# Performance work log

Measured on AMD Instinct MI355X. Metric: run time of the kernel, lower is better.

The kernel has to match this reference:

```python
import jax, jax.numpy as jnp
import numpy as np

K_NEIGHBORS = 8

def _cdist(x, y):
    x2 = jnp.sum(x * x, axis=-1)[:, None]
    y2 = jnp.sum(y * y, axis=-1)[None, :]
    d2 = x2 + y2 - 2.0 * (x @ y.T)
    return jnp.sqrt(jnp.maximum(d2, 0.0))

def setup_inputs() -> dict:
    key = jax.random.key(0)
    ks = jax.random.split(key, 16)
    B, C, H, W = 8, 384, 64, 64
    s = lambda fan: 1.0 / np.sqrt(fan)
    inp = {
        'fea': jax.random.normal(ks[0], (B, C, H, W), dtype=jnp.float32),
        # GCNConv weights (applied as x @ W) and post-aggregation biases
        'W1': jax.random.normal(ks[1], (C, C), jnp.float32) * s(C),
        'b1': jnp.zeros((C,), jnp.float32),
        'W2': jax.random.normal(ks[2], (C, C), jnp.float32) * s(C),
        'b2': jnp.zeros((C,), jnp.float32),
        'W3': jax.random.normal(ks[3], (C, C), jnp.float32) * s(C),
        'b3': jnp.zeros((C,), jnp.float32),
        # uncertainty MLP: C -> C/2 -> C/4 -> 1
        'U1': jax.random.normal(ks[4], (C, C // 2), jnp.float32) * s(C),
        'ub1': jnp.zeros((C // 2,), jnp.float32),
        'U2': jax.random.normal(ks[5], (C // 2, C // 4), jnp.float32) * s(C // 2),
        'ub2': jnp.zeros((C // 4,), jnp.float32),
        'U3': jax.random.normal(ks[6], (C // 4, 1), jnp.float32) * s(C // 4),
        'ub3': jnp.zeros((1,), jnp.float32),
    }
    return inp

def _build_graph(fea, k):
    B, C, H, W = fea.shape
    N = H * W
    gy, gx = jnp.meshgrid(jnp.arange(H), jnp.arange(W), indexing='ij')
    coord = jnp.stack([gy, gx], axis=-1).astype(jnp.float32).reshape(N, 2)
    fea_mean = fea.reshape(B, C, N).transpose(0, 2, 1).mean(0)  # [N, C]
    spatial_dist = _cdist(coord, coord)
    feature_dist = _cdist(fea_mean, fea_mean)
    combined = 0.7 * spatial_dist + 0.3 * feature_dist
    _, topk_idx = jax.lax.top_k(-combined, k)  # smallest-k per row
    src = jnp.repeat(jnp.arange(N), k)         # edge_index[0]
    dst = topk_idx.reshape(-1)                 # edge_index[1]
    return src, dst, N

def _gcn_conv(x, W, b, src, dst, N):
    # PyG GCNConv with symmetric normalization; self-loops are guaranteed
    # by construction (diag of combined dist is 0, strictly minimal), so
    # add_remaining_self_loops is a no-op.
    xw = x @ W                                              # [B, N, C]
    deg = jnp.zeros((N,), x.dtype).at[dst].add(1.0)
    dinv = jax.lax.rsqrt(deg)
    norm = dinv[src] * dinv[dst]                            # [E]
    msgs = xw[:, src, :] * norm[None, :, None]              # [B, E, C]
    out = jnp.zeros_like(xw).at[:, dst, :].add(msgs)
    return out + b

def reference(fea, W1, b1, W2, b2, W3, b3, U1, ub1, U2, ub2, U3, ub3):
    B, C, H, W = fea.shape
    src, dst, N = _build_graph(fea, K_NEIGHBORS)
    x = fea.reshape(B, C, N).transpose(0, 2, 1)             # [B, N, C]
    x = x + jax.nn.relu(_gcn_conv(x, W1, b1, src, dst, N))
    x = x + jax.nn.relu(_gcn_conv(x, W2, b2, src, dst, N))
    x = x + jax.nn.relu(_gcn_conv(x, W3, b3, src, dst, N))
    h = jax.nn.gelu(x @ U1 + ub1)
    h = jax.nn.gelu(h @ U2 + ub2)
    unc = jax.nn.sigmoid(h @ U3 + ub3)                      # [B, N, 1]
    unc = unc.reshape(B, 1, H, W)
    return fea * (1.0 + unc)
```

## Files before the change

### kernel.cpp

```cpp
#include <hip/hip_runtime.h>
#include <hip/hip_bf16.h>
#include <math.h>

#define N_NODES 4096
#define C_DIM   384
#define B_DIM   8
#define K_NB    8
#define E_TOT   (N_NODES * K_NB)
#define M_ROWS  (B_DIM * N_NODES)
#define NCHUNK  4
#define SROW    40

typedef unsigned long long u64;
typedef unsigned short u16;
typedef __attribute__((ext_vector_type(8))) short bf16x8;
typedef __attribute__((ext_vector_type(4))) float f32x4;
#define KEY_INF 0xFFFFFFFFFFFFFFFFull

__device__ __forceinline__ u16 f2bf(float f) {
  unsigned u = __float_as_uint(f);
  u += 0x7FFFu + ((u >> 16) & 1u);
  return (u16)(u >> 16);
}
__device__ __forceinline__ float bf2f(u16 h) {
  return __uint_as_float((unsigned)h << 16);
}
__device__ __forceinline__ f32x4 mfma16(bf16x8 a, bf16x8 b, f32x4 c) {
  return __builtin_amdgcn_mfma_f32_16x16x32_bf16(a, b, c, 0, 0, 0);
}
__device__ __forceinline__ void gl_lds16(const u16* gp, u16* lp) {
  __builtin_amdgcn_global_load_lds(
      (const __attribute__((address_space(1))) unsigned int*)gp,
      (__attribute__((address_space(3))) unsigned int*)lp, 16, 0, 0);
}

__device__ __forceinline__ void ce(u64& a, u64& b) {
  u64 lo = a < b ? a : b;
  u64 hi = a < b ? b : a;
  a = lo; b = hi;
}
__device__ __forceinline__ void ins8(u64 key, u64 (&r)[8]) {
  if (key < r[7]) {
    #pragma unroll
    for (int i = 0; i < 8; i++) {
      u64 lo = key < r[i] ? key : r[i];
      u64 hi = key < r[i] ? r[i] : key;
      r[i] = lo; key = hi;
    }
  }
}
__device__ __forceinline__ void merge8(u64 (&r)[8], const u64 (&o)[8]) {
  u64 c[8];
  #pragma unroll
  for (int i = 0; i < 8; i++) c[i] = r[i] < o[7 - i] ? r[i] : o[7 - i];
  ce(c[0], c[4]); ce(c[1], c[5]); ce(c[2], c[6]); ce(c[3], c[7]);
  ce(c[0], c[2]); ce(c[1], c[3]); ce(c[4], c[6]); ce(c[5], c[7]);
  ce(c[0], c[1]); ce(c[2], c[3]); ce(c[4], c[5]); ce(c[6], c[7]);
  #pragma unroll
  for (int i = 0; i < 8; i++) r[i] = c[i];
}

__global__ __launch_bounds__(256) void k_prep_w(
    const float* __restrict__ W1, const float* __restrict__ W2,
    const float* __restrict__ W3, const float* __restrict__ U1,
    const float* __restrict__ U2,
    u16* __restrict__ Wt1, u16* __restrict__ Wt2, u16* __restrict__ Wt3,
    u16* __restrict__ U1t, u16* __restrict__ U2t) {
  int idx = blockIdx.x * 256 + threadIdx.x;
  if (idx < 147456) {
    int n = idx / 384, k = idx % 384;
    Wt1[idx] = f2bf(W1[k * 384 + n]);
  } else if (idx < 294912) {
    int i = idx - 147456; int n = i / 384, k = i % 384;
    Wt2[i] = f2bf(W2[k * 384 + n]);
  } else if (idx < 442368) {
    int i = idx - 294912; int n = i / 384, k = i % 384;
    Wt3[i] = f2bf(W3[k * 384 + n]);
  } else if (idx < 516096) {
    int i = idx - 442368; int n = i / 384, k = i % 384;
    U1t[i] = f2bf(U1[k * 192 + n]);
  } else if (idx < 534528) {
    int i = idx - 516096; int n = i / 192, k = i % 192;
    U2t[i] = f2bf(U2[k * 96 + n]);
  }
}

__global__ __launch_bounds__(256) void k_transpose_mean(
    const float* __restrict__ fea, u16* __restrict__ Xb,
    u16* __restrict__ fh, u16* __restrict__ fl) {
  __shared__ float tb[32][132];
  __shared__ float ac[32][132];
  int n0 = blockIdx.x * 128, c0 = blockIdx.y * 32;
  int tx = threadIdx.x, ty = threadIdx.y;
  for (int i = ty; i < 32; i += 8) {
    #pragma unroll
    for (int e = 0; e < 4; e++) ac[i][tx * 4 + e] = 0.0f;
  }
  __syncthreads();
  for (int b = 0; b < B_DIM; b++) {
    for (int i = ty; i < 32; i += 8) {
      float4 v = *(const float4*)(fea +
          ((size_t)b * C_DIM + (c0 + i)) * N_NODES + n0 + tx * 4);
      *(float4*)&tb[i][tx * 4] = v;
      ac[i][tx * 4 + 0] += v.x;
      ac[i][tx * 4 + 1] += v.y;
      ac[i][tx * 4 + 2] += v.z;
      ac[i][tx * 4 + 3] += v.w;
    }
    __syncthreads();
    for (int rr = ty; rr < 128; rr += 8) {
      size_t o = ((size_t)b * N_NODES + (n0 + rr)) * C_DIM + c0 + tx;
      Xb[o] = f2bf(tb[tx][rr]);
    }
    __syncthreads();
  }
  for (int rr = ty; rr < 128; rr += 8) {
    float m = ac[tx][rr] * 0.125f;
    u16 h = f2bf(m);
    size_t o = (size_t)(n0 + rr) * C_DIM + c0 + tx;
    fh[o] = h;
    fl[o] = f2bf(m - bf2f(h));
  }
}

__global__ __launch_bounds__(64) void k_x2(const u16* __restrict__ fh,
                                           const u16* __restrict__ fl,
                                           float* __restrict__ x2) {
  int n = blockIdx.x;
  int lane = threadIdx.x;
  const u16* rh = fh + (size_t)n * C_DIM;
  const u16* rl = fl + (size_t)n * C_DIM;
  float s = 0.0f;
  for (int c = lane; c < C_DIM; c += 64) {
    float v = bf2f(rh[c]) + bf2f(rl[c]);
    s += v * v;
  }
  for (int d = 32; d > 0; d >>= 1) s += __shfl_down(s, d);
  if (lane == 0) x2[n] = s;
}

__global__ __launch_bounds__(256) void k_dist_win(
    const u16* __restrict__ fh, const u16* __restrict__ fl,
    const float* __restrict__ x2, u64* __restrict__ pk,
    int* __restrict__ deg, int* __restrict__ cnt) {
  __shared__ u16 WH[400 * SROW];
  __shared__ u16 WL[400 * SROW];
  int t = threadIdx.x;
  int lane = t & 63, w = t >> 6;
  int p = blockIdx.x;
  int py = p >> 4, px = p & 15;
  int iy0 = py * 4, ix0 = px * 4;
  int l15 = lane & 15;
  int kb = (lane >> 4) * 8;

  if (p < 16) { deg[p * 256 + t] = 0; cnt[p * 256 + t] = 0; }

  int t0 = (w == 0) ? 0 : 7 + (w - 1) * 6;
  int nt = w ? 6 : 7;

  int jj[7]; float x2j[7]; int jy_[7], jx_[7];
  #pragma unroll
  for (int tt = 0; tt < 7; tt++) {
    int s = (t0 + tt) * 16 + l15;
    int sy = s / 20, sx = s - sy * 20;
    int jy = iy0 - 8 + sy, jx = ix0 - 8 + sx;
    bool v = (tt < nt) && ((unsigned)jy < 64u) && ((unsigned)jx < 64u);
    jj[tt] = v ? (jy * 64 + jx) : -1;
    jy_[tt] = jy; jx_[tt] = jx;
    x2j[tt] = v ? x2[jy * 64 + jx] : 0.0f;
  }
  int pr = 168 + (l15 >> 2) * 20 + (l15 & 3);

  int seg = t & 3;
  int rb = t >> 2;

  f32x4 acc[7];
  #pragma unroll
  for (int tt = 0; tt < 7; tt++) acc[tt] = (f32x4){0.f, 0.f, 0.f, 0.f};

  for (int kc = 0; kc < 12; kc++) {
    int k0 = kc * 32;
    __syncthreads();
    #pragma unroll
    for (int it = 0; it < 7; it++) {
      int r = rb + 64 * it;
      if (r < 400) {
        int sy = r / 20, sx = r - sy * 20;
        int jy = iy0 - 8 + sy, jx = ix0 - 8 + sx;
        int j = (((unsigned)jy < 64u) && ((unsigned)jx < 64u)) ? jy * 64 + jx : 0;
        size_t src = (size_t)j * C_DIM + k0 + seg * 8;
        *(bf16x8*)&WH[r * SROW + seg * 8] = *(const bf16x8*)(fh + src);
        *(bf16x8*)&WL[r * SROW + seg * 8] = *(const bf16x8*)(fl + src);
      }
    }
    __syncthreads();
    bf16x8 aH = *(const bf16x8*)&WH[pr * SROW + kb];
    bf16x8 aL = *(const bf16x8*)&WL[pr * SROW + kb];
    #pragma unroll
    for (int tt = 0; tt < 7; tt++) {
      int row = (t0 + tt) * 16 + l15;
      bf16x8 bH = *(const bf16x8*)&WH[row * SROW + kb];
      bf16x8 bL = *(const bf16x8*)&WL[row * SROW + kb];
      acc[tt] = mfma16(aH, bH, acc[tt]);
      acc[tt] = mfma16(aL, bH, acc[tt]);
      acc[tt] = mfma16(aH, bL, acc[tt]);
    }
  }

  #pragma unroll
  for (int r = 0; r < 4; r++) {
    int r16 = ((lane >> 4) << 2) + r;
    int iy = iy0 + (r16 >> 2), ix = ix0 + (r16 & 3);
    int i = iy * 64 + ix;
    float x2i = x2[i];
    u64 top[8];
    #pragma unroll
    for (int q = 0; q < 8; q++) top[q] = KEY_INF;
    #pragma unroll
    for (int tt = 0; tt < 7; tt++) {
      float d2 = x2i + x2j[tt] - 2.0f * acc[tt][r];
      float fd = sqrtf(fmaxf(d2, 0.0f));
      float dy = (float)(iy - jy_[tt]), dx = (float)(ix - jx_[tt]);
      float sd = sqrtf(dy * dy + dx * dx);
      float comb = 0.7f * sd + 0.3f * fd;
      u64 key = (jj[tt] >= 0)
                    ? (((u64)__float_as_uint(comb) << 12) | (u64)jj[tt])
                    : KEY_INF;
      ins8(key, top);
    }
    #pragma unroll
    for (int d = 1; d < 16; d <<= 1) {
      u64 o[8];
      #pragma unroll
      for (int q = 0; q < 8; q++) o[q] = __shfl_xor(top[q], d);
      merge8(top, o);
    }
    if (l15 == 0) {
      #pragma unroll
      for (int q = 0; q < 8; q++)
        pk[((size_t)w * N_NODES + i) * 8 + q] = top[q];
    }
  }
}

__global__ __launch_bounds__(256) void k_topk_merge(
    const u64* __restrict__ pk, int* __restrict__ tk, int* __restrict__ flag,
    int* __restrict__ deg) {
  int n = blockIdx.x * 256 + threadIdx.x;
  if (n >= N_NODES) return;
  u64 r[8];
  #pragma unroll
  for (int q = 0; q < 8; q++) r[q] = KEY_INF;
  for (int c = 0; c < NCHUNK; c++) {
    const u64* lst = pk + ((size_t)c * N_NODES + n) * 8;
    #pragma unroll
    for (int q = 0; q < 8; q++) {
      u64 key = lst[q];
      if (key >= r[7]) break;
      ins8(key, r);
    }
  }
  float c8 = __uint_as_float((unsigned)(r[7] >> 12));
  int fl = (c8 > 6.28f) ? 1 : 0;
  flag[n] = fl;
  #pragma unroll
  for (int o = 0; o < 8; o++) {
    int idx = (int)(r[o] & 0xFFF);
    tk[n * 8 + o] = idx;
    if (!fl) atomicAdd(&deg[idx], 1);
  }
}

__global__ __launch_bounds__(256) void k_fb(
    const u16* __restrict__ fh, const u16* __restrict__ fl,
    const float* __restrict__ x2, const int* __restrict__ flag,
    int* __restrict__ tk, int* __restrict__ deg) {
  int w = threadIdx.x >> 6, lane = threadIdx.x & 63;
  for (int rr = 0; rr < 16; rr++) {
    int n = blockIdx.x * 64 + w * 16 + rr;
    if (!flag[n]) continue;
    u64 top[8];
    #pragma unroll
    for (int q = 0; q < 8; q++) top[q] = KEY_INF;
    float x2i = x2[n];
    int iy = n >> 6, ix = n & 63;
    const u16* rh = fh + (size_t)n * C_DIM;
    const u16* rl = fl + (size_t)n * C_DIM;
    for (int jb = 0; jb < N_NODES; jb += 64) {
      int j = jb + lane;
      const u16* ch = fh + (size_t)j * C_DIM;
      const u16* cl = fl + (size_t)j * C_DIM;
      float dot = 0.0f;
      for (int k2 = 0; k2 < C_DIM; k2++)
        dot += (bf2f(rh[k2]) + bf2f(rl[k2])) * (bf2f(ch[k2]) + bf2f(cl[k2]));
      float d2 = x2i + x2[j] - 2.0f * dot;
      float fd = sqrtf(fmaxf(d2, 0.0f));
      float dy = (float)(iy - (j >> 6)), dx = (float)(ix - (j & 63));
      float sd = sqrtf(dy * dy + dx * dx);
      float comb = 0.7f * sd + 0.3f * fd;
      ins8(((u64)__float_as_uint(comb) << 12) | (u64)j, top);
    }
    #pragma unroll
    for (int d = 1; d < 64; d <<= 1) {
      u64 o[8];
      #pragma unroll
      for (int q = 0; q < 8; q++) o[q] = __shfl_xor(top[q], d);
      merge8(top, o);
    }
    if (lane == 0) {
      #pragma unroll
      for (int q = 0; q < 8; q++) {
        int idx = (int)(top[q] & 0xFFF);
        tk[n * 8 + q] = idx;
        atomicAdd(&deg[idx], 1);
      }
    }
  }
}

__global__ __launch_bounds__(256) void k_scan(const int* __restrict__ deg,
                                              int* __restrict__ offs,
                                              float* __restrict__ dinv) {
  __shared__ int ps[256];
  int t = threadIdx.x;
  int base = t * 16;
  int loc[16]; int s = 0;
  for (int i = 0; i < 16; i++) { int d = deg[base + i]; loc[i] = s; s += d; }
  ps[t] = s;
  __syncthreads();
  for (int d = 1; d < 256; d <<= 1) {
    int add = (t >= d) ? ps[t - d] : 0;
    __syncthreads();
    ps[t] += add;
    __syncthreads();
  }
  int cbase = (t == 0) ? 0 : ps[t - 1];
  for (int i = 0; i < 16; i++) offs[base + i] = cbase + loc[i];
  if (t == 255) offs[N_NODES] = ps[255];
  for (int i = 0; i < 16; i++)
    dinv[base + i] = 1.0f / sqrtf((float)deg[base + i]);
}

__global__ __launch_bounds__(256) void k_fill(const int* __restrict__ tk,
                                              const int* __restrict__ offs,
                                              int* __restrict__ cnt,
                                              int* __restrict__ insrc) {
  int e = blockIdx.x * 256 + threadIdx.x;
  if (e >= E_TOT) return;
  int i = e >> 3;
  int n = tk[e];
  int pos = offs[n] + atomicAdd(&cnt[n], 1);
  insrc[pos] = i;
}

__global__ __launch_bounds__(256) void k_sort(const int* __restrict__ offs,
                                              int* __restrict__ insrc) {
  int n = blockIdx.x * 256 + threadIdx.x;
  if (n >= N_NODES) return;
  int beg = offs[n], end = offs[n + 1];
  for (int a = beg + 1; a < end; a++) {
    int v = insrc[a]; int p = a;
    while (p > beg && insrc[p - 1] > v) { insrc[p] = insrc[p - 1]; p--; }
    insrc[p] = v;
  }
}

__device__ __forceinline__ float gelu_f(float x) {
  const float k0 = 0.7978845608028654f;
  float x3 = x * x * x;
  return 0.5f * x * (1.0f + tanhf(k0 * (x + 0.044715f * x3)));
}

template <int EPI>
__global__ __launch_bounds__(256) void k_gemm_lds(
    const u16* __restrict__ A, const u16* __restrict__ Bt,
    const float* __restrict__ bias, u16* __restrict__ Cout,
    int M, int N, int K) {
  __shared__ u16 As[128 * 32];
  __shared__ u16 Bs[128 * 32];
  int t = threadIdx.x, lane = t & 63, w = t >> 6;
  int m0 = blockIdx.x * 128;
  int n0 = blockIdx.y * 128;
  int l15 = lane & 15;
  int kg = lane >> 4;
  int wr = (w >> 1) * 64, wc = (w & 1) * 64;

  int srow = w * 32 + (lane >> 2);
  int scol = (lane & 3) * 8;
  const u16* gA0 = A + (size_t)(m0 + srow) * K + scol;
  const u16* gA1 = A + (size_t)(m0 + srow + 16) * K + scol;
  int br0 = n0 + srow;      br0 = (br0 < N) ? br0 : 0;
  int br1 = n0 + srow + 16; br1 = (br1 < N) ? br1 : 0;
  const u16* gB0 = Bt + (size_t)br0 * K + scol;
  const u16* gB1 = Bt + (size_t)br1 * K + scol;
  u16* lA0 = &As[(w * 32) * 32];
  u16* lA1 = &As[(w * 32 + 16) * 32];
  u16* lB0 = &Bs[(w * 32) * 32];
  u16* lB1 = &Bs[(w * 32 + 16) * 32];

  f32x4 acc[4][4];
  #pragma unroll
  for (int s = 0; s < 4; s++)
    #pragma unroll
    for (int nt = 0; nt < 4; nt++) acc[s][nt] = (f32x4){0.f, 0.f, 0.f, 0.f};

  for (int kt = 0; kt < K; kt += 32) {
    __syncthreads();
    gl_lds16(gA0 + kt, lA0);
    gl_lds16(gA1 + kt, lA1);
    gl_lds16(gB0 + kt, lB0);
    gl_lds16(gB1 + kt, lB1);
    __syncthreads();
    bf16x8 a[4], b[4];
    #pragma unroll
    for (int s = 0; s < 4; s++)
      a[s] = *(const bf16x8*)&As[(wr + s * 16 + l15) * 32 + kg * 8];
    #pragma unroll
    for (int nt = 0; nt < 4; nt++)
      b[nt] = *(const bf16x8*)&Bs[(wc + nt * 16 + l15) * 32 + kg * 8];
    #pragma unroll
    for (int s = 0; s < 4; s++)
      #pragma unroll
      for (int nt = 0; nt < 4; nt++)
        acc[s][nt] = mfma16(a[s], b[nt], acc[s][nt]);
  }

  #pragma unroll
  for (int s = 0; s < 4; s++) {
    int rbase = m0 + wr + s * 16 + ((lane >> 4) << 2);
    #pragma unroll
    for (int nt = 0; nt < 4; nt++) {
      int n = n0 + wc + nt * 16 + l15;
      if (n >= N) continue;
      float bb = (EPI == 1) ? bias[n] : 0.0f;
      #pragma unroll
      for (int r = 0; r < 4; r++) {
        int m = rbase + r;
        float v = acc[s][nt][r];
        if (EPI == 1) { v += bb; v = gelu_f(v); }
        Cout[(size_t)m * N + n] = f2bf(v);
      }
    }
  }
}

__global__ __launch_bounds__(256) void k_mlp2(
    const u16* __restrict__ A, const u16* __restrict__ Bt,
    const float* __restrict__ ub2, const float* __restrict__ U3,
    const float* __restrict__ ub3, float* __restrict__ unc) {
  const int K = 192;
  int t = threadIdx.x, lane = t & 63, w = t >> 6;
  int m0 = blockIdx.x * 128 + w * 32;
  int l15 = lane & 15;
  int kb = (lane >> 4) * 8;

  f32x4 acc[2][6];
  #pragma unroll
  for (int s = 0; s < 2; s++)
    #pragma unroll
    for (int nt = 0; nt < 6; nt++) acc[s][nt] = (f32x4){0.f, 0.f, 0.f, 0.f};

  const u16* ap = A + (size_t)(m0 + l15) * K + kb;
  const u16* bp[6];
  #pragma unroll
  for (int nt = 0; nt < 6; nt++)
    bp[nt] = Bt + (size_t)(nt * 16 + l15) * K + kb;
  const size_t RA = (size_t)16 * K;

  #pragma unroll
  for (int kk = 0; kk < K; kk += 32) {
    bf16x8 a[2], b[6];
    #pragma unroll
    for (int s = 0; s < 2; s++) a[s] = *(const bf16x8*)(ap + s * RA + kk);
    #pragma unroll
    for (int nt = 0; nt < 6; nt++) b[nt] = *(const bf16x8*)(bp[nt] + kk);
    #pragma unroll
    for (int s = 0; s < 2; s++)
      #pragma unroll
      for (int nt = 0; nt < 6; nt++)
        acc[s][nt] = mfma16(a[s], b[nt], acc[s][nt]);
  }

  float ub3v = ub3[0];
  float u3v[6], b2v[6];
  #pragma unroll
  for (int nt = 0; nt < 6; nt++) {
    int col = nt * 16 + l15;
    u3v[nt] = U3[col];
    b2v[nt] = ub2[col];
  }
  #pragma unroll
  for (int s = 0; s < 2; s++) {
    #pragma unroll
    for (int r = 0; r < 4; r++) {
      float part = 0.0f;
      #pragma unroll
      for (int nt = 0; nt < 6; nt++)
        part += gelu_f(acc[s][nt][r] + b2v[nt]) * u3v[nt];
      #pragma unroll
      for (int d = 1; d < 16; d <<= 1) part += __shfl_xor(part, d);
      if (l15 == 0) {
        int m = m0 + s * 16 + ((lane >> 4) << 2) + r;
        unc[m] = 1.0f / (1.0f + expf(-(part + ub3v)));
      }
    }
  }
}

__global__ __launch_bounds__(384) void k_gcn_agg(
    const u16* __restrict__ xw, u16* __restrict__ Xb,
    const float* __restrict__ bias, const float* __restrict__ dinv,
    const int* __restrict__ offs, const int* __restrict__ insrc) {
  const size_t PLANE = (size_t)N_NODES * C_DIM;
  int t = threadIdx.x;
  int g = t / 48, l = t % 48;
  int slot = blockIdx.x * 8 + g;
  int n = slot >> 1;
  int hb = (slot & 1) * 4;
  int beg = offs[n], end = offs[n + 1];
  int c0 = l * 8;
  const u16* base = xw + c0 + (size_t)hb * PLANE;

  float a0[8] = {}, a1[8] = {}, a2[8] = {}, a3[8] = {};
  for (int e = beg; e < end; e++) {
    int i = insrc[e];
    float dv = dinv[i];
    const u16* rp = base + (size_t)i * C_DIM;
    bf16x8 v0 = *(const bf16x8*)(rp);
    bf16x8 v1 = *(const bf16x8*)(rp + PLANE);
    bf16x8 v2 = *(const bf16x8*)(rp + 2 * PLANE);
    bf16x8 v3 = *(const bf16x8*)(rp + 3 * PLANE);
    #pragma unroll
    for (int ch = 0; ch < 8; ch++) {
      a0[ch] += dv * bf2f((u16)v0[ch]);
      a1[ch] += dv * bf2f((u16)v1[ch]);
      a2[ch] += dv * bf2f((u16)v2[ch]);
      a3[ch] += dv * bf2f((u16)v3[ch]);
    }
  }

  float dn = dinv[n];
  float bv[8];
  #pragma unroll
  for (int ch = 0; ch < 8; ch++) bv[ch] = bias[c0 + ch];
  size_t ob = (size_t)n * C_DIM + c0 + (size_t)hb * PLANE;
  u16* xp0 = Xb + ob;
  u16* xp1 = Xb + ob + PLANE;
  u16* xp2 = Xb + ob + 2 * PLANE;
  u16* xp3 = Xb + ob + 3 * PLANE;
  bf16x8 xo0 = *(const bf16x8*)xp0, xo1 = *(const bf16x8*)xp1;
  bf16x8 xo2 = *(const bf16x8*)xp2, xo3 = *(const bf16x8*)xp3;
  bf16x8 xn0, xn1, xn2, xn3;
  #pragma unroll
  for (int ch = 0; ch < 8; ch++) {
    xn0[ch] = (short)f2bf(bf2f((u16)xo0[ch]) + fmaxf(dn * a0[ch] + bv[ch], 0.f));
    xn1[ch] = (short)f2bf(bf2f((u16)xo1[ch]) + fmaxf(dn * a1[ch] + bv[ch], 0.f));
    xn2[ch] = (short)f2bf(bf2f((u16)xo2[ch]) + fmaxf(dn * a2[ch] + bv[ch], 0.f));
    xn3[ch] = (short)f2bf(bf2f((u16)xo3[ch]) + fmaxf(dn * a3[ch] + bv[ch], 0.f));
  }
  *(bf16x8*)xp0 = xn0;
  *(bf16x8*)xp1 = xn1;
  *(bf16x8*)xp2 = xn2;
  *(bf16x8*)xp3 = xn3;
}

__global__ __launch_bounds__(256) void k_final(
    const float* __restrict__ fea, const float* __restrict__ unc,
    float* __restrict__ out) {
  size_t i4 = (size_t)blockIdx.x * 256 + threadIdx.x;
  size_t idx = i4 * 4;
  if (idx >= (size_t)B_DIM * C_DIM * N_NODES) return;
  int b = (int)(idx / ((size_t)C_DIM * N_NODES));
  int n = (int)(idx & (N_NODES - 1));
  float4 f = *(const float4*)(fea + idx);
  float4 u = *(const float4*)(unc + (size_t)b * N_NODES + n);
  float4 o;
  o.x = f.x * (1.0f + u.x);
  o.y = f.y * (1.0f + u.y);
  o.z = f.z * (1.0f + u.z);
  o.w = f.w * (1.0f + u.w);
  *(float4*)(out + idx) = o;
}

extern "C" void kernel_launch(void* const* d_in, const int* in_sizes, int n_in,
                              void* d_out, int out_size, void* d_ws, size_t ws_size,
                              hipStream_t stream) {
  const float* fea = (const float*)d_in[0];
  const float* W1  = (const float*)d_in[1];
  const float* b1  = (const float*)d_in[2];
  const float* W2  = (const float*)d_in[3];
  const float* b2  = (const float*)d_in[4];
  const float* W3  = (const float*)d_in[5];
  const float* b3  = (const float*)d_in[6];
  const float* U1  = (const float*)d_in[7];
  const float* ub1 = (const float*)d_in[8];
  const float* U2  = (const float*)d_in[9];
  const float* ub2 = (const float*)d_in[10];
  const float* U3  = (const float*)d_in[11];
  const float* ub3 = (const float*)d_in[12];
  float* out = (float*)d_out;

  char* ws = (char*)d_ws;
  u16*   Xb   = (u16*)  (ws + 0);
  u16*   XWb  = (u16*)  (ws + 25165824);
  u64*   pk   = (u64*)  (ws + 25165824);
  u16*   h1b  = (u16*)  (ws + 25165824);
  u16*   fh   = (u16*)  (ws + 50331648);
  u16*   fl   = (u16*)  (ws + 53477376);
  float* x2   = (float*)(ws + 56623104);
  int*   tk   = (int*)  (ws + 56639488);
  int*   deg  = (int*)  (ws + 56770560);
  float* dinv = (float*)(ws + 56786944);
  int*   offs = (int*)  (ws + 56803328);
  int*   cnt  = (int*)  (ws + 56820224);
  int*   insrc= (int*)  (ws + 56836608);
  float* unc  = (float*)(ws + 56967680);
  u16*   Wt1  = (u16*)  (ws + 57098752);
  u16*   Wt2  = (u16*)  (ws + 57393664);
  u16*   Wt3  = (u16*)  (ws + 57688576);
  u16*   U1t  = (u16*)  (ws + 57983488);
  u16*   U2t  = (u16*)  (ws + 58130944);
  int*   flag = (int*)  (ws + 58167808);

  k_prep_w<<<2088, 256, 0, stream>>>(W1, W2, W3, U1, U2, Wt1, Wt2, Wt3, U1t, U2t);
  k_transpose_mean<<<dim3(N_NODES / 128, C_DIM / 32), dim3(32, 8), 0, stream>>>(
      fea, Xb, fh, fl);
  k_x2<<<N_NODES, 64, 0, stream>>>(fh, fl, x2);
  k_dist_win<<<256, 256, 0, stream>>>(fh, fl, x2, pk, deg, cnt);
  k_topk_merge<<<N_NODES / 256, 256, 0, stream>>>(pk, tk, flag, deg);
  k_fb<<<64, 256, 0, stream>>>(fh, fl, x2, flag, tk, deg);
  k_scan<<<1, 256, 0, stream>>>(deg, offs, dinv);
  k_fill<<<E_TOT / 256, 256, 0, stream>>>(tk, offs, cnt, insrc);
  k_sort<<<N_NODES / 256, 256, 0, stream>>>(offs, insrc);
  const u16* Wl[3] = {Wt1, Wt2, Wt3};
  const float* bl[3] = {b1, b2, b3};
  for (int l = 0; l < 3; l++) {
    k_gemm_lds<3><<<dim3(M_ROWS / 128, 3), 256, 0, stream>>>(
        Xb, Wl[l], nullptr, XWb, M_ROWS, C_DIM, C_DIM);
    k_gcn_agg<<<N_NODES / 4, 384, 0, stream>>>(XWb, Xb, bl[l], dinv, offs, insrc);
  }
  k_gemm_lds<1><<<dim3(M_ROWS / 128, 2), 256, 0, stream>>>(
      Xb, U1t, ub1, h1b, M_ROWS, 192, C_DIM);
  k_mlp2<<<M_ROWS / 128, 256, 0, stream>>>(h1b, U2t, ub2, U3, ub3, unc);
  size_t tot = (size_t)B_DIM * C_DIM * N_NODES;
  k_final<<<(tot / 4 + 255) / 256, 256, 0, stream>>>(fea, unc, out);
}
```

Baseline: 281.1 us.

## Vectorize transpose stores, fuse topk merge with fallback, double-buffer GEMM LDS

Three separate changes. The transpose/mean kernel now writes 8 bf16 values per 16-byte store instead of scalar 2-byte stores. The top-k merge and brute-force fallback kernels are fused into one launch that compacts flagged rows into a shared list, which removes a launch and the flag buffer and gives the fallback 16 blocks instead of 64. The GEMM uses double-buffered LDS so the next K tile's global-to-LDS load is issued while the current tile's MFMAs run, dropping one barrier per iteration at the cost of twice the LDS.

```diff
diff --git a/kernel.cpp b/kernel.cpp
--- a/kernel.cpp
+++ b/kernel.cpp
@@ -92,6 +92,9 @@
   __shared__ float ac[32][132];
   int n0 = blockIdx.x * 128, c0 = blockIdx.y * 32;
   int tx = threadIdx.x, ty = threadIdx.y;
+  int flat = ty * 32 + tx;
+  int g = flat & 3;
+  int r2 = flat >> 2;
   for (int i = ty; i < 32; i += 8) {
     #pragma unroll
     for (int e = 0; e < 4; e++) ac[i][tx * 4 + e] = 0.0f;
@@ -108,18 +111,30 @@
       ac[i][tx * 4 + 3] += v.w;
     }
     __syncthreads();
-    for (int rr = ty; rr < 128; rr += 8) {
-      size_t o = ((size_t)b * N_NODES + (n0 + rr)) * C_DIM + c0 + tx;
-      Xb[o] = f2bf(tb[tx][rr]);
+    #pragma unroll
+    for (int half = 0; half < 2; half++) {
+      int r = r2 + 64 * half;
+      bf16x8 v;
+      #pragma unroll
+      for (int cc = 0; cc < 8; cc++) v[cc] = (short)f2bf(tb[g * 8 + cc][r]);
+      *(bf16x8*)&Xb[((size_t)b * N_NODES + n0 + r) * C_DIM + c0 + g * 8] = v;
     }
     __syncthreads();
   }
-  for (int rr = ty; rr < 128; rr += 8) {
-    float m = ac[tx][rr] * 0.125f;
-    u16 h = f2bf(m);
-    size_t o = (size_t)(n0 + rr) * C_DIM + c0 + tx;
-    fh[o] = h;
-    fl[o] = f2bf(m - bf2f(h));
+  #pragma unroll
+  for (int half = 0; half < 2; half++) {
+    int r = r2 + 64 * half;
+    bf16x8 vh, vl;
+    #pragma unroll
+    for (int cc = 0; cc < 8; cc++) {
+      float m = ac[g * 8 + cc][r] * 0.125f;
+      u16 h = f2bf(m);
+      vh[cc] = (short)h;
+      vl[cc] = (short)f2bf(m - bf2f(h));
+    }
+    size_t o = (size_t)(n0 + r) * C_DIM + c0 + g * 8;
+    *(bf16x8*)&fh[o] = vh;
+    *(bf16x8*)&fl[o] = vl;
   }
 }
 
@@ -243,49 +258,54 @@
   }
 }
 
-__global__ __launch_bounds__(256) void k_topk_merge(
-    const u64* __restrict__ pk, int* __restrict__ tk, int* __restrict__ flag,
-    int* __restrict__ deg) {
-  int n = blockIdx.x * 256 + threadIdx.x;
-  if (n >= N_NODES) return;
-  u64 r[8];
-  #pragma unroll
-  for (int q = 0; q < 8; q++) r[q] = KEY_INF;
-  for (int c = 0; c < NCHUNK; c++) {
-    const u64* lst = pk + ((size_t)c * N_NODES + n) * 8;
-    #pragma unroll
-    for (int q = 0; q < 8; q++) {
-      u64 key = lst[q];
-      if (key >= r[7]) break;
-      ins8(key, r);
-    }
-  }
-  float c8 = __uint_as_float((unsigned)(r[7] >> 12));
-  int fl = (c8 > 6.28f) ? 1 : 0;
-  flag[n] = fl;
-  #pragma unroll
-  for (int o = 0; o < 8; o++) {
-    int idx = (int)(r[o] & 0xFFF);
-    tk[n * 8 + o] = idx;
-    if (!fl) atomicAdd(&deg[idx], 1);
-  }
-}
-
-__global__ __launch_bounds__(256) void k_fb(
-    const u16* __restrict__ fh, const u16* __restrict__ fl,
-    const float* __restrict__ x2, const int* __restrict__ flag,
+__global__ __launch_bounds__(256) void k_topk_merge_fb(
+    const u64* __restrict__ pk, const u16* __restrict__ fh,
+    const u16* __restrict__ fl, const float* __restrict__ x2,
     int* __restrict__ tk, int* __restrict__ deg) {
-  int w = threadIdx.x >> 6, lane = threadIdx.x & 63;
-  for (int rr = 0; rr < 16; rr++) {
-    int n = blockIdx.x * 64 + w * 16 + rr;
-    if (!flag[n]) continue;
+  __shared__ int fl_list[256];
+  __shared__ int fl_cnt;
+  int t = threadIdx.x;
+  if (t == 0) fl_cnt = 0;
+  __syncthreads();
+  int n = blockIdx.x * 256 + t;
+  {
+    u64 r[8];
+    #pragma unroll
+    for (int q = 0; q < 8; q++) r[q] = KEY_INF;
+    for (int c = 0; c < NCHUNK; c++) {
+      const u64* lst = pk + ((size_t)c * N_NODES + n) * 8;
+      #pragma unroll
+      for (int q = 0; q < 8; q++) {
+        u64 key = lst[q];
+        if (key >= r[7]) break;
+        ins8(key, r);
+      }
+    }
+    float c8 = __uint_as_float((unsigned)(r[7] >> 12));
+    if (c8 > 6.28f) {
+      int pos = atomicAdd(&fl_cnt, 1);
+      fl_list[pos] = n;
+    } else {
+      #pragma unroll
+      for (int o = 0; o < 8; o++) {
+        int idx = (int)(r[o] & 0xFFF);
+        tk[n * 8 + o] = idx;
+        atomicAdd(&deg[idx], 1);
+      }
+    }
+  }
+  __syncthreads();
+  int nf = fl_cnt;
+  int w = t >> 6, lane = t & 63;
+  for (int fi = w; fi < nf; fi += 4) {
+    int nn = fl_list[fi];
     u64 top[8];
     #pragma unroll
     for (int q = 0; q < 8; q++) top[q] = KEY_INF;
-    float x2i = x2[n];
-    int iy = n >> 6, ix = n & 63;
-    const u16* rh = fh + (size_t)n * C_DIM;
-    const u16* rl = fl + (size_t)n * C_DIM;
+    float x2i = x2[nn];
+    int iy = nn >> 6, ix = nn & 63;
+    const u16* rh = fh + (size_t)nn * C_DIM;
+    const u16* rl = fl + (size_t)nn * C_DIM;
     for (int jb = 0; jb < N_NODES; jb += 64) {
       int j = jb + lane;
       const u16* ch = fh + (size_t)j * C_DIM;
@@ -311,7 +331,7 @@
       #pragma unroll
       for (int q = 0; q < 8; q++) {
         int idx = (int)(top[q] & 0xFFF);
-        tk[n * 8 + q] = idx;
+        tk[nn * 8 + q] = idx;
         atomicAdd(&deg[idx], 1);
       }
     }
@@ -376,8 +396,9 @@
     const u16* __restrict__ A, const u16* __restrict__ Bt,
     const float* __restrict__ bias, u16* __restrict__ Cout,
     int M, int N, int K) {
-  __shared__ u16 As[128 * 32];
-  __shared__ u16 Bs[128 * 32];
+  __shared__ u16 As[2 * 128 * 32];
+  __shared__ u16 Bs[2 * 128 * 32];
+  const int BO = 128 * 32;
   int t = threadIdx.x, lane = t & 63, w = t >> 6;
   int m0 = blockIdx.x * 128;
   int n0 = blockIdx.y * 128;
@@ -393,10 +414,8 @@
   int br1 = n0 + srow + 16; br1 = (br1 < N) ? br1 : 0;
   const u16* gB0 = Bt + (size_t)br0 * K + scol;
   const u16* gB1 = Bt + (size_t)br1 * K + scol;
-  u16* lA0 = &As[(w * 32) * 32];
-  u16* lA1 = &As[(w * 32 + 16) * 32];
-  u16* lB0 = &Bs[(w * 32) * 32];
-  u16* lB1 = &Bs[(w * 32 + 16) * 32];
+  int lo0 = (w * 32) * 32;
+  int lo1 = (w * 32 + 16) * 32;
 
   f32x4 acc[4][4];
   #pragma unroll
@@ -404,25 +423,36 @@
     #pragma unroll
     for (int nt = 0; nt < 4; nt++) acc[s][nt] = (f32x4){0.f, 0.f, 0.f, 0.f};
 
-  for (int kt = 0; kt < K; kt += 32) {
-    __syncthreads();
-    gl_lds16(gA0 + kt, lA0);
-    gl_lds16(gA1 + kt, lA1);
-    gl_lds16(gB0 + kt, lB0);
-    gl_lds16(gB1 + kt, lB1);
-    __syncthreads();
+  gl_lds16(gA0, &As[lo0]);
+  gl_lds16(gA1, &As[lo1]);
+  gl_lds16(gB0, &Bs[lo0]);
+  gl_lds16(gB1, &Bs[lo1]);
+  __syncthreads();
+
+  int NT = K / 32;
+  for (int kt = 0; kt < NT; kt++) {
+    int cur = (kt & 1) * BO;
+    if (kt + 1 < NT) {
+      int nb = ((kt + 1) & 1) * BO;
+      int ko = (kt + 1) * 32;
+      gl_lds16(gA0 + ko, &As[nb + lo0]);
+      gl_lds16(gA1 + ko, &As[nb + lo1]);
+      gl_lds16(gB0 + ko, &Bs[nb + lo0]);
+      gl_lds16(gB1 + ko, &Bs[nb + lo1]);
+    }
     bf16x8 a[4], b[4];
     #pragma unroll
     for (int s = 0; s < 4; s++)
-      a[s] = *(const bf16x8*)&As[(wr + s * 16 + l15) * 32 + kg * 8];
+      a[s] = *(const bf16x8*)&As[cur + (wr + s * 16 + l15) * 32 + kg * 8];
     #pragma unroll
     for (int nt = 0; nt < 4; nt++)
-      b[nt] = *(const bf16x8*)&Bs[(wc + nt * 16 + l15) * 32 + kg * 8];
+      b[nt] = *(const bf16x8*)&Bs[cur + (wc + nt * 16 + l15) * 32 + kg * 8];
     #pragma unroll
     for (int s = 0; s < 4; s++)
       #pragma unroll
       for (int nt = 0; nt < 4; nt++)
         acc[s][nt] = mfma16(a[s], b[nt], acc[s][nt]);
+    if (kt + 1 < NT) __syncthreads();
   }
 
   #pragma unroll
@@ -620,15 +650,13 @@
   u16*   Wt3  = (u16*)  (ws + 57688576);
   u16*   U1t  = (u16*)  (ws + 57983488);
   u16*   U2t  = (u16*)  (ws + 58130944);
-  int*   flag = (int*)  (ws + 58167808);
 
   k_prep_w<<<2088, 256, 0, stream>>>(W1, W2, W3, U1, U2, Wt1, Wt2, Wt3, U1t, U2t);
   k_transpose_mean<<<dim3(N_NODES / 128, C_DIM / 32), dim3(32, 8), 0, stream>>>(
       fea, Xb, fh, fl);
   k_x2<<<N_NODES, 64, 0, stream>>>(fh, fl, x2);
   k_dist_win<<<256, 256, 0, stream>>>(fh, fl, x2, pk, deg, cnt);
-  k_topk_merge<<<N_NODES / 256, 256, 0, stream>>>(pk, tk, flag, deg);
-  k_fb<<<64, 256, 0, stream>>>(fh, fl, x2, flag, tk, deg);
+  k_topk_merge_fb<<<N_NODES / 256, 256, 0, stream>>>(pk, fh, fl, x2, tk, deg);
   k_scan<<<1, 256, 0, stream>>>(deg, offs, dinv);
   k_fill<<<E_TOT / 256, 256, 0, stream>>>(tk, offs, cnt, insrc);
   k_sort<<<N_NODES / 256, 256, 0, stream>>>(offs, insrc);
```

New measurement: 273.4 us. -2.7%, faster.
